# Optimization experiments

Hardware: AMD Instinct MI355X
Metric: run time of the kernel (lower is better)

Reference implementation:

```python
import jax, jax.numpy as jnp
import numpy as np

B, L, P, A = 32, 512, 128, 128   # batch, prot seq len, prot dim, atom dim
N = 1024                          # total atoms (32 per molecule)
H1, H2 = 512, 256                 # hidden_list


def setup_inputs() -> dict:
    key = jax.random.key(0)
    ks = jax.random.split(key, 12)
    atom_embed = jax.random.normal(ks[0], (N, A), dtype=jnp.float32)
    protSeq_embed = jax.random.normal(ks[1], (B, L, P), dtype=jnp.float32)
    # sorted segment ids, every segment non-empty (32 atoms per molecule)
    atom_splits = jnp.repeat(jnp.arange(B, dtype=jnp.int64), N // B)
    s = 0.05
    att1_W = jax.random.normal(ks[2], (P + A, 128), dtype=jnp.float32) * s
    att1_b = jnp.zeros((128,), dtype=jnp.float32)
    att2_W = jax.random.normal(ks[3], (128, 1), dtype=jnp.float32) * s
    att2_b = jnp.zeros((1,), dtype=jnp.float32)
    d1_W = jax.random.normal(ks[4], (A + P, H1), dtype=jnp.float32) * s
    d1_b = jnp.zeros((H1,), dtype=jnp.float32)
    d2_W = jax.random.normal(ks[5], (H1, H2), dtype=jnp.float32) * s
    d2_b = jnp.zeros((H2,), dtype=jnp.float32)
    out_W = jax.random.normal(ks[6], (H2, 1), dtype=jnp.float32) * s
    out_b = jnp.zeros((1,), dtype=jnp.float32)
    return {"atom_embed": atom_embed, "protSeq_embed": protSeq_embed,
            "atom_splits": atom_splits,
            "att1_W": att1_W, "att1_b": att1_b, "att2_W": att2_W, "att2_b": att2_b,
            "d1_W": d1_W, "d1_b": d1_b, "d2_W": d2_W, "d2_b": d2_b,
            "out_W": out_W, "out_b": out_b}


def reference(atom_embed, protSeq_embed, atom_splits,
              att1_W, att1_b, att2_W, att2_b,
              d1_W, d1_b, d2_W, d2_b, out_W, out_b):
    num_seg = protSeq_embed.shape[0]
    # gather protein rows per atom: [N, L, P]
    prot_g = protSeq_embed[atom_splits]
    # concat with broadcast atom embed: [N, L, P+A]
    atom_x = jnp.broadcast_to(atom_embed[:, None, :], prot_g.shape[:2] + atom_embed.shape[-1:])
    concat = jnp.concatenate([prot_g, atom_x], axis=-1)
    # attention MLP -> scores W: [N, L]
    hid = jnp.tanh(concat @ att1_W + att1_b)
    W = 5.0 * jnp.tanh(hid @ att2_W + att2_b)[..., 0]
    # atom-side weights: exp(max over seq), normalized per segment
    Wc = jnp.exp(jnp.max(W, axis=-1, keepdims=True))                     # [N, 1]
    Sc = jax.ops.segment_sum(Wc, atom_splits, num_segments=num_seg)[atom_splits]
    aa = Wc / Sc                                                          # [N, 1]
    atom_pool = jax.ops.segment_sum(aa * atom_embed, atom_splits, num_segments=num_seg)  # [B, A]
    # protein-side: segment-max scores, softmax over seq, weighted sum
    Wp = jax.ops.segment_max(W, atom_splits, num_segments=num_seg)       # [B, L]
    ap = jax.nn.softmax(Wp, axis=-1)
    prot_pool = jnp.einsum('bl,bld->bd', ap, protSeq_embed)              # [B, P]
    z = jnp.concatenate([atom_pool, prot_pool], axis=-1)
    z = jax.nn.relu(z @ d1_W + d1_b)
    z = jax.nn.relu(z @ d2_W + d2_b)
    return z @ out_W + out_b                                             # [B, 1]
```

## Files before the change

kernel.cpp:

```cpp
#include <hip/hip_runtime.h>
#include <math.h>

#define BSEG 32
#define LSEQ 512

__device__ __forceinline__ float fast_tanh(float x) {
    x = fminf(fmaxf(x, -20.0f), 20.0f);
    float e = __expf(2.0f * x);
    return __fdividef(e - 1.0f, e + 1.0f);
}
__device__ __forceinline__ float trm(float c, float p, float e) {
    return c * __builtin_amdgcn_rcpf(fmaf(p, e, 1.0f));
}
__device__ __forceinline__ float clexp2(float v) {
    return __expf(2.0f * fminf(fmaxf(v, -20.0f), 20.0f));
}

__device__ __forceinline__ void gemm32_exp(
    const float* __restrict__ Xrow0, const float* __restrict__ Wm,
    const float* __restrict__ bias, float* __restrict__ xs,
    float* __restrict__ ws, float* __restrict__ dst, int tid)
{
    #pragma unroll
    for (int t = 0; t < 4; ++t) {
        int flat = (tid + 256 * t) * 4;
        int r = flat >> 7, k4 = flat & 127;
        *(float4*)&xs[r * 132 + k4] = *(const float4*)&Xrow0[r * 128 + k4];
    }
    const int tx = tid & 31, ty = tid >> 5;
    float acc[4][4];
    #pragma unroll
    for (int i = 0; i < 4; ++i)
        #pragma unroll
        for (int j = 0; j < 4; ++j) acc[i][j] = 0.0f;
    #pragma unroll
    for (int q = 0; q < 4; ++q) {
        #pragma unroll
        for (int t = 0; t < 4; ++t) {
            int flat = (tid + 256 * t) * 4;
            int kk = flat >> 7, c4 = flat & 127;
            *(float4*)&ws[kk * 132 + c4] =
                *(const float4*)&Wm[(q * 32 + kk) * 128 + c4];
        }
        __syncthreads();
        #pragma unroll 4
        for (int kk = 0; kk < 32; ++kk) {
            float4 b4 = *(const float4*)&ws[kk * 132 + 4 * tx];
            int k = q * 32 + kk;
            float a0 = xs[(4 * ty + 0) * 132 + k];
            float a1 = xs[(4 * ty + 1) * 132 + k];
            float a2 = xs[(4 * ty + 2) * 132 + k];
            float a3 = xs[(4 * ty + 3) * 132 + k];
            acc[0][0] += a0 * b4.x; acc[0][1] += a0 * b4.y;
            acc[0][2] += a0 * b4.z; acc[0][3] += a0 * b4.w;
            acc[1][0] += a1 * b4.x; acc[1][1] += a1 * b4.y;
            acc[1][2] += a1 * b4.z; acc[1][3] += a1 * b4.w;
            acc[2][0] += a2 * b4.x; acc[2][1] += a2 * b4.y;
            acc[2][2] += a2 * b4.z; acc[2][3] += a2 * b4.w;
            acc[3][0] += a3 * b4.x; acc[3][1] += a3 * b4.y;
            acc[3][2] += a3 * b4.z; acc[3][3] += a3 * b4.w;
        }
        __syncthreads();
    }
    float b4v[4] = {0.f, 0.f, 0.f, 0.f};
    if (bias) *(float4*)b4v = *(const float4*)&bias[4 * tx];
    #pragma unroll
    for (int i = 0; i < 4; ++i) {
        float4 o;
        o.x = clexp2(acc[i][0] + b4v[0]);
        o.y = clexp2(acc[i][1] + b4v[1]);
        o.z = clexp2(acc[i][2] + b4v[2]);
        o.w = clexp2(acc[i][3] + b4v[3]);
        *(float4*)&dst[(4 * ty + i) * 132 + 4 * tx] = o;
    }
}

__global__ __launch_bounds__(256, 2) void fused_kernel(
    const float* __restrict__ atom_embed, const float* __restrict__ protSeq,
    const float* __restrict__ att1_W, const float* __restrict__ att1_b,
    const float* __restrict__ att2_W, const float* __restrict__ att2_b,
    const float* __restrict__ out_b,
    float* __restrict__ pmax, float* __restrict__ zrp,
    float* __restrict__ dpp, float* __restrict__ out)
{
    __shared__ float smem[16896];
    float* eps = smem;
    float* ebs = smem + 4224;
    float* xs  = smem + 8448;
    float* ws  = smem + 12672;
    float* c_s  = smem + 8448;
    float* pmn  = smem + 8576;
    float* wps  = smem + 9664;
    float* es   = smem + 9696;
    float* part = smem + 9728;
    float* scal = smem + 9984;

    const int tid = threadIdx.x;
    const int chunk = blockIdx.x, b = blockIdx.y;
    const int lbase = chunk * 32;

    if (chunk == 0 && tid == 0) out[b] = out_b[0];

    gemm32_exp(protSeq + ((long)(b * 512 + lbase)) * 128, att1_W, att1_b,
               xs, ws, eps, tid);
    gemm32_exp(atom_embed + (long)b * 32 * 128, att1_W + 128 * 128, nullptr,
               xs, ws, ebs, tid);

    if (tid < 128) c_s[tid] = -2.0f * att2_W[tid];
    __syncthreads();
    if (tid < 64) {
        float s = c_s[tid] + c_s[tid + 64];
        #pragma unroll
        for (int m = 1; m < 64; m <<= 1) s += __shfl_xor(s, m);
        if (tid == 0) scal[0] = -0.5f * s + att2_b[0];
    }
    __syncthreads();

    const int ng = tid & 7, lg = tid >> 3;
    const float* qp  = &eps[lg * 132];
    const float* b0p = &ebs[ng * 132];
    const float* b1p = &ebs[(ng + 8) * 132];
    const float* b2p = &ebs[(ng + 16) * 132];
    const float* b3p = &ebs[(ng + 24) * 132];
    float a0 = 0.f, a1 = 0.f, a2 = 0.f, a3 = 0.f;
    #pragma unroll 4
    for (int jj = 0; jj < 128; jj += 4) {
        float4 c4 = *(const float4*)&c_s[jj];
        float4 q  = *(const float4*)(qp + jj);
        float4 b0 = *(const float4*)(b0p + jj);
        float4 b1 = *(const float4*)(b1p + jj);
        float4 b2 = *(const float4*)(b2p + jj);
        float4 b3 = *(const float4*)(b3p + jj);
        a0 += trm(c4.x, q.x, b0.x); a1 += trm(c4.x, q.x, b1.x);
        a2 += trm(c4.x, q.x, b2.x); a3 += trm(c4.x, q.x, b3.x);
        a0 += trm(c4.y, q.y, b0.y); a1 += trm(c4.y, q.y, b1.y);
        a2 += trm(c4.y, q.y, b2.y); a3 += trm(c4.y, q.y, b3.y);
        a0 += trm(c4.z, q.z, b0.z); a1 += trm(c4.z, q.z, b1.z);
        a2 += trm(c4.z, q.z, b2.z); a3 += trm(c4.z, q.z, b3.z);
        a0 += trm(c4.w, q.w, b0.w); a1 += trm(c4.w, q.w, b1.w);
        a2 += trm(c4.w, q.w, b2.w); a3 += trm(c4.w, q.w, b3.w);
    }
    const float bs = scal[0];
    float W0 = 5.0f * fast_tanh(a0 + bs);
    float W1 = 5.0f * fast_tanh(a1 + bs);
    float W2 = 5.0f * fast_tanh(a2 + bs);
    float W3 = 5.0f * fast_tanh(a3 + bs);

    float m = fmaxf(fmaxf(W0, W1), fmaxf(W2, W3));
    #pragma unroll
    for (int d = 1; d < 8; d <<= 1) m = fmaxf(m, __shfl_xor(m, d));
    if (ng == 0) wps[lg] = m;
    pmn[lg * 34 + ng]      = W0;
    pmn[lg * 34 + ng + 8]  = W1;
    pmn[lg * 34 + ng + 16] = W2;
    pmn[lg * 34 + ng + 24] = W3;
    __syncthreads();
    if (tid < 32) {
        float mm = pmn[tid];
        #pragma unroll
        for (int g = 1; g < 32; ++g) mm = fmaxf(mm, pmn[g * 34 + tid]);
        pmax[b * 512 + chunk * 32 + tid] = mm;
        es[tid] = __expf(wps[tid]);
    }
    __syncthreads();
    if (tid < 32) {
        float v = es[tid];
        #pragma unroll
        for (int d = 1; d < 32; d <<= 1) v += __shfl_xor(v, d);
        if (tid == 0) dpp[b * 16 + chunk] = v;
    }
    const int dd = tid & 127, hf = tid >> 7;
    float az = 0.0f;
    #pragma unroll 4
    for (int i = 0; i < 16; ++i)
        az += es[hf * 16 + i] *
              protSeq[((long)(b * 512 + lbase + hf * 16 + i)) * 128 + dd];
    part[tid] = az;
    __syncthreads();
    if (tid < 128) zrp[(b * 16 + chunk) * 128 + tid] = part[tid] + part[128 + tid];
}

__global__ __launch_bounds__(256) void tail_kernel(
    const float* __restrict__ pmax, const float* __restrict__ zrp,
    const float* __restrict__ dpp, const float* __restrict__ atom_embed,
    const float* __restrict__ d1_W, const float* __restrict__ d1_b,
    const float* __restrict__ d2_W, const float* __restrict__ d2_b,
    const float* __restrict__ out_W, float* __restrict__ out)
{
    __shared__ float zs[256];
    __shared__ float hs[512];
    __shared__ float expw[32];
    __shared__ float part[8 * 33];
    __shared__ float sc[2];
    const int tid = threadIdx.x;
    const int cx = blockIdx.x, b = blockIdx.y;

    if (tid < 32) {
        float m = -1e30f;
        #pragma unroll
        for (int c = 0; c < 16; ++c) m = fmaxf(m, pmax[b * 512 + c * 32 + tid]);
        float e = __expf(m);
        expw[tid] = e;
        #pragma unroll
        for (int d = 1; d < 32; d <<= 1) e += __shfl_xor(e, d);
        if (tid == 0) sc[0] = 1.0f / e;
    }
    if (tid == 64) {
        float s = 0.0f;
        #pragma unroll
        for (int c = 0; c < 16; ++c) s += dpp[b * 16 + c];
        sc[1] = 1.0f / s;
    }
    __syncthreads();
    if (tid < 128) {
        float a = 0.0f;
        #pragma unroll 4
        for (int n = 0; n < 32; ++n)
            a += expw[n] * atom_embed[(b * 32 + n) * 128 + tid];
        zs[tid] = a * sc[0];
    } else {
        int d = tid - 128;
        float a = 0.0f;
        #pragma unroll
        for (int c = 0; c < 16; ++c) a += zrp[(b * 16 + c) * 128 + d];
        zs[tid] = a * sc[1];
    }
    __syncthreads();

    #pragma unroll
    for (int rep = 0; rep < 2; ++rep) {
        int c = tid + 256 * rep;
        float a = d1_b[c];
        #pragma unroll 8
        for (int k = 0; k < 256; ++k) a += zs[k] * d1_W[k * 512 + c];
        hs[c] = fmaxf(a, 0.0f);
    }
    __syncthreads();

    const int c0 = cx * 32, ci = tid & 31, kg = tid >> 5;
    float a2 = 0.0f;
    #pragma unroll 8
    for (int k = kg * 64; k < kg * 64 + 64; ++k)
        a2 += hs[k] * d2_W[k * 256 + c0 + ci];
    part[kg * 33 + ci] = a2;
    __syncthreads();
    if (tid < 32) {
        float s = d2_b[c0 + tid];
        #pragma unroll
        for (int g = 0; g < 8; ++g) s += part[g * 33 + tid];
        float contrib = fmaxf(s, 0.0f) * out_W[c0 + tid];
        #pragma unroll
        for (int d = 1; d < 32; d <<= 1) contrib += __shfl_xor(contrib, d);
        if (tid == 0) atomicAdd(&out[b], contrib);
    }
}

extern "C" void kernel_launch(void* const* d_in, const int* in_sizes, int n_in,
                              void* d_out, int out_size, void* d_ws, size_t ws_size,
                              hipStream_t stream) {
    const float* atom_embed = (const float*)d_in[0];
    const float* protSeq    = (const float*)d_in[1];
    const float* att1_W = (const float*)d_in[3];
    const float* att1_b = (const float*)d_in[4];
    const float* att2_W = (const float*)d_in[5];
    const float* att2_b = (const float*)d_in[6];
    const float* d1_W   = (const float*)d_in[7];
    const float* d1_b   = (const float*)d_in[8];
    const float* d2_W   = (const float*)d_in[9];
    const float* d2_b   = (const float*)d_in[10];
    const float* out_W  = (const float*)d_in[11];
    const float* out_b  = (const float*)d_in[12];
    float* out = (float*)d_out;

    float* ws = (float*)d_ws;
    float* pmax = ws;
    float* zrp  = pmax + 16384;
    float* dpp  = zrp + 65536;

    fused_kernel<<<dim3(16, BSEG), 256, 0, stream>>>(
        atom_embed, protSeq, att1_W, att1_b, att2_W, att2_b, out_b,
        pmax, zrp, dpp, out);
    tail_kernel<<<dim3(8, BSEG), 256, 0, stream>>>(
        pmax, zrp, dpp, atom_embed, d1_W, d1_b, d2_W, d2_b, out_W, out);
}
```

Baseline: 142.8 us.

## Split MLP tail into two kernels to remove redundant first-layer compute

The tail kernel previously recomputed the full 512-wide first dense layer in every column block of each batch row. The work is now split into two kernels. The first computes a 64-column slice of layer one per block, using a split-k reduction in shared memory, and writes the hidden activations to workspace. The second loads them and does layer two plus the output projection. This removes the 8x redundant d1 computation at the cost of an extra kernel launch and a global round trip for the hidden vector.

```diff
diff --git a/kernel.cpp b/kernel.cpp
--- a/kernel.cpp
+++ b/kernel.cpp
@@ -180,17 +180,15 @@
     if (tid < 128) zrp[(b * 16 + chunk) * 128 + tid] = part[tid] + part[128 + tid];
 }
 
-__global__ __launch_bounds__(256) void tail_kernel(
+__global__ __launch_bounds__(256) void mlp1_kernel(
     const float* __restrict__ pmax, const float* __restrict__ zrp,
     const float* __restrict__ dpp, const float* __restrict__ atom_embed,
     const float* __restrict__ d1_W, const float* __restrict__ d1_b,
-    const float* __restrict__ d2_W, const float* __restrict__ d2_b,
-    const float* __restrict__ out_W, float* __restrict__ out)
+    float* __restrict__ h1)
 {
     __shared__ float zs[256];
-    __shared__ float hs[512];
+    __shared__ float part[4 * 65];
     __shared__ float expw[32];
-    __shared__ float part[8 * 33];
     __shared__ float sc[2];
     const int tid = threadIdx.x;
     const int cx = blockIdx.x, b = blockIdx.y;
@@ -214,7 +212,7 @@
     __syncthreads();
     if (tid < 128) {
         float a = 0.0f;
-        #pragma unroll 4
+        #pragma unroll 8
         for (int n = 0; n < 32; ++n)
             a += expw[n] * atom_embed[(b * 32 + n) * 128 + tid];
         zs[tid] = a * sc[0];
@@ -226,23 +224,38 @@
         zs[tid] = a * sc[1];
     }
     __syncthreads();
-
-    #pragma unroll
-    for (int rep = 0; rep < 2; ++rep) {
-        int c = tid + 256 * rep;
-        float a = d1_b[c];
-        #pragma unroll 8
-        for (int k = 0; k < 256; ++k) a += zs[k] * d1_W[k * 512 + c];
-        hs[c] = fmaxf(a, 0.0f);
-    }
-    __syncthreads();
-
-    const int c0 = cx * 32, ci = tid & 31, kg = tid >> 5;
-    float a2 = 0.0f;
+    const int c0 = cx * 64, ci = tid & 63, kg = tid >> 6;
+    float acc = 0.0f;
     #pragma unroll 8
     for (int k = kg * 64; k < kg * 64 + 64; ++k)
-        a2 += hs[k] * d2_W[k * 256 + c0 + ci];
-    part[kg * 33 + ci] = a2;
+        acc += zs[k] * d1_W[k * 512 + c0 + ci];
+    part[kg * 65 + ci] = acc;
+    __syncthreads();
+    if (tid < 64) {
+        float s = part[tid] + part[65 + tid] + part[130 + tid] + part[195 + tid]
+                + d1_b[c0 + tid];
+        h1[b * 512 + c0 + tid] = fmaxf(s, 0.0f);
+    }
+}
+
+__global__ __launch_bounds__(256) void mlp2_kernel(
+    const float* __restrict__ h1, const float* __restrict__ d2_W,
+    const float* __restrict__ d2_b, const float* __restrict__ out_W,
+    float* __restrict__ out)
+{
+    __shared__ float hs[512];
+    __shared__ float part[8 * 33];
+    const int tid = threadIdx.x;
+    const int c0 = blockIdx.x * 32, b = blockIdx.y;
+    hs[tid] = h1[b * 512 + tid];
+    hs[tid + 256] = h1[b * 512 + 256 + tid];
+    __syncthreads();
+    const int ci = tid & 31, kg = tid >> 5;
+    float acc = 0.0f;
+    #pragma unroll 8
+    for (int k = kg * 64; k < kg * 64 + 64; ++k)
+        acc += hs[k] * d2_W[k * 256 + c0 + ci];
+    part[kg * 33 + ci] = acc;
     __syncthreads();
     if (tid < 32) {
         float s = d2_b[c0 + tid];
@@ -276,10 +289,13 @@
     float* pmax = ws;
     float* zrp  = pmax + 16384;
     float* dpp  = zrp + 65536;
+    float* h1   = dpp + 512;
 
     fused_kernel<<<dim3(16, BSEG), 256, 0, stream>>>(
         atom_embed, protSeq, att1_W, att1_b, att2_W, att2_b, out_b,
         pmax, zrp, dpp, out);
-    tail_kernel<<<dim3(8, BSEG), 256, 0, stream>>>(
-        pmax, zrp, dpp, atom_embed, d1_W, d1_b, d2_W, d2_b, out_W, out);
-}
+    mlp1_kernel<<<dim3(8, BSEG), 256, 0, stream>>>(
+        pmax, zrp, dpp, atom_embed, d1_W, d1_b, h1);
+    mlp2_kernel<<<dim3(8, BSEG), 256, 0, stream>>>(
+        h1, d2_W, d2_b, out_W, out);
+}
```

Result: faster. 123.9 us (-13.2%).
